# Kernel optimization log

Measured on AMD Instinct MI355X. Metric: run time of the kernel, lower is better.

The kernel has to match this reference:

```python
import jax, jax.numpy as jnp
import numpy as np
import math

B, TT, TS, C, H, L = 8, 256, 512, 512, 8, 10
HD = C // H
TOPK_FRAME = 64
# layer schedule mirrors MultimodalTransformer.forward tower order:
# 4 stimulus cross-attn (kv=frames, topk), 2 causal self-attn, 2 history cross-attn, 2 causal self-attn
# kv_source: 0=frames, 1=self, 2=id_prev
SCHED = [(0, False, TOPK_FRAME)] * 4 + [(1, True, None)] * 2 + [(2, False, None)] * 2 + [(1, True, None)] * 2


def setup_inputs() -> dict:
    key = jax.random.key(0)
    ks = jax.random.split(key, 4)
    kws = jax.random.split(ks[3], 6)
    w = lambda k, s: jax.random.normal(k, s, jnp.float32) * 0.02
    return {
        "id_x": jax.random.normal(ks[0], (B, TT, C), jnp.float32),
        "id_prev": jax.random.normal(ks[1], (B, TT, C), jnp.float32),
        "frames": jax.random.normal(ks[2], (B, TS, C), jnp.float32),
        "Wq": w(kws[0], (L, C, C)), "bq": jnp.zeros((L, C), jnp.float32),
        "Wk": w(kws[1], (L, C, C)), "bk": jnp.zeros((L, C), jnp.float32),
        "Wv": w(kws[2], (L, C, C)), "bv": jnp.zeros((L, C), jnp.float32),
        "Wo": w(kws[3], (L, C, C)), "bo": jnp.zeros((L, C), jnp.float32),
        "W1": w(kws[4], (L, C, 4 * C)), "b1": jnp.zeros((L, 4 * C), jnp.float32),
        "W2": w(kws[5], (L, 4 * C, C)), "b2": jnp.zeros((L, C), jnp.float32),
        "ln1_g": jnp.ones((L, C), jnp.float32), "ln1_b": jnp.zeros((L, C), jnp.float32),
        "ln2_g": jnp.ones((L, C), jnp.float32), "ln2_b": jnp.zeros((L, C), jnp.float32),
        "lnf_g": jnp.ones((L, C), jnp.float32), "lnf_b": jnp.zeros((L, C), jnp.float32),
    }


def _ln(x, g, b):
    mu = x.mean(-1, keepdims=True)
    var = ((x - mu) ** 2).mean(-1, keepdims=True)
    return (x - mu) * jax.lax.rsqrt(var + 1e-5) * g + b


def _block(x, kv, causal, topk, p):
    # Block.forward: x = x + attn(ln1(x), kv, kv, mask); x = x + mlp(ln2(x)); return ln_f(x)
    Wq, bq, Wk, bk, Wv, bv, Wo, bo, W1, b1, W2, b2, l1g, l1b, l2g, l2b, lfg, lfb = p
    Bx, Tt, Cx = x.shape
    Ts = kv.shape[1]
    h = _ln(x, l1g, l1b)
    q = (h @ Wq + bq).reshape(Bx, Tt, H, HD).transpose(0, 2, 1, 3)   # [B,H,Tt,HD]
    k = (kv @ Wk + bk).reshape(Bx, Ts, H, HD).transpose(0, 2, 1, 3)  # [B,H,Ts,HD]
    v = (kv @ Wv + bv).reshape(Bx, Ts, H, HD).transpose(0, 2, 1, 3)
    att = jnp.einsum('bhqd,bhkd->bhqk', q, k) * (1.0 / math.sqrt(HD))
    if causal:
        m = jnp.tril(jnp.ones((Tt, Ts), dtype=bool))
        att = jnp.where(m, att, -jnp.inf)
    if topk is not None and topk < Ts:
        top = jax.lax.top_k(att, topk)[0]           # [B,H,Tt,topk]
        att = jnp.where(att < top[..., -1:], -jnp.inf, att)
    w_att = jax.nn.softmax(att, axis=-1)
    y = jnp.einsum('bhqk,bhkd->bhqd', w_att, v).transpose(0, 2, 1, 3).reshape(Bx, Tt, Cx)
    x = x + y @ Wo + bo
    h2 = _ln(x, l2g, l2b)
    x = x + jax.nn.gelu(h2 @ W1 + b1, approximate=False) @ W2 + b2
    return _ln(x, lfg, lfb)


def _forward(id_x, id_prev, frames, Wq, bq, Wk, bk, Wv, bv, Wo, bo, W1, b1, W2, b2,
             ln1_g, ln1_b, ln2_g, ln2_b, lnf_g, lnf_b):
    x = id_x
    for i, (src, causal, topk) in enumerate(SCHED):
        kv = (frames, x, id_prev)[src]
        p = (Wq[i], bq[i], Wk[i], bk[i], Wv[i], bv[i], Wo[i], bo[i],
             W1[i], b1[i], W2[i], b2[i],
             ln1_g[i], ln1_b[i], ln2_g[i], ln2_b[i], lnf_g[i], lnf_b[i])
        x = _block(x, kv, causal, topk, p)
    return x


def reference(id_x, id_prev, frames, Wq, bq, Wk, bk, Wv, bv, Wo, bo, W1, b1, W2, b2,
              ln1_g, ln1_b, ln2_g, ln2_b, lnf_g, lnf_b):
    return _forward(id_x, id_prev, frames, Wq, bq, Wk, bk, Wv, bv, Wo, bo, W1, b1, W2, b2,
                    ln1_g, ln1_b, ln2_g, ln2_b, lnf_g, lnf_b)
```

## Files before the change

### kernel.cpp

```cpp
#include <hip/hip_runtime.h>
#include <math.h>

#define CC 512
#define NH 8
#define HD 64
#define TT 256

typedef __attribute__((ext_vector_type(8))) short short8v;
typedef __attribute__((ext_vector_type(4))) float f32x4;

__device__ inline unsigned short bfc(float f) {
  unsigned u = __float_as_uint(f);
  return (unsigned short)((u + 0x7fffu + ((u >> 16) & 1u)) >> 16);
}
__device__ inline float b2f(unsigned short s) {
  return __uint_as_float((unsigned)s << 16);
}
__device__ inline void gld16(const void* g, void* l) {
  __builtin_amdgcn_global_load_lds(
      (const __attribute__((address_space(1))) unsigned int*)g,
      (__attribute__((address_space(3))) unsigned int*)l, 16, 0, 0);
}

__global__ __launch_bounds__(256) void prep_k(const float* __restrict__ id_x,
    const float* __restrict__ frames, const float* __restrict__ id_prev,
    float* __restrict__ x, unsigned short* __restrict__ fb,
    unsigned short* __restrict__ pb) {
  int i = blockIdx.x * 256 + threadIdx.x;
  if (i < 262144) {
    ((float4*)x)[i] = ((const float4*)id_x)[i];
  } else if (i < 786432) {
    int j = i - 262144;
    float4 f = ((const float4*)frames)[j];
    ushort4 o; o.x = bfc(f.x); o.y = bfc(f.y); o.z = bfc(f.z); o.w = bfc(f.w);
    ((ushort4*)fb)[j] = o;
  } else {
    int j = i - 786432;
    float4 f = ((const float4*)id_prev)[j];
    ushort4 o; o.x = bfc(f.x); o.y = bfc(f.y); o.z = bfc(f.z); o.w = bfc(f.w);
    ((ushort4*)pb)[j] = o;
  }
}

__global__ __launch_bounds__(256) void ln_bf(const float* __restrict__ in,
    unsigned short* __restrict__ out, const float* __restrict__ g, const float* __restrict__ b) {
  int row = (blockIdx.x << 2) + (threadIdx.x >> 6), lane = threadIdx.x & 63;
  const float* r = in + (size_t)row * CC;
  float4 v0 = *(const float4*)(r + (lane << 2));
  float4 v1 = *(const float4*)(r + 256 + (lane << 2));
  float s = v0.x + v0.y + v0.z + v0.w + v1.x + v1.y + v1.z + v1.w;
  #pragma unroll
  for (int o = 32; o; o >>= 1) s += __shfl_xor(s, o);
  float mu = s * (1.0f / CC);
  float d0x = v0.x - mu, d0y = v0.y - mu, d0z = v0.z - mu, d0w = v0.w - mu;
  float d1x = v1.x - mu, d1y = v1.y - mu, d1z = v1.z - mu, d1w = v1.w - mu;
  float sq = d0x*d0x + d0y*d0y + d0z*d0z + d0w*d0w + d1x*d1x + d1y*d1y + d1z*d1z + d1w*d1w;
  #pragma unroll
  for (int o = 32; o; o >>= 1) sq += __shfl_xor(sq, o);
  float inv = rsqrtf(sq * (1.0f / CC) + 1e-5f);
  float4 g0 = *(const float4*)(g + (lane << 2)), g1 = *(const float4*)(g + 256 + (lane << 2));
  float4 b0 = *(const float4*)(b + (lane << 2)), b1 = *(const float4*)(b + 256 + (lane << 2));
  ushort4 o0, o1;
  o0.x = bfc(d0x*inv*g0.x + b0.x); o0.y = bfc(d0y*inv*g0.y + b0.y);
  o0.z = bfc(d0z*inv*g0.z + b0.z); o0.w = bfc(d0w*inv*g0.w + b0.w);
  o1.x = bfc(d1x*inv*g1.x + b1.x); o1.y = bfc(d1y*inv*g1.y + b1.y);
  o1.z = bfc(d1z*inv*g1.z + b1.z); o1.w = bfc(d1w*inv*g1.w + b1.w);
  *(ushort4*)(out + (size_t)row * CC + (lane << 2)) = o0;
  *(ushort4*)(out + (size_t)row * CC + 256 + (lane << 2)) = o1;
}

__global__ __launch_bounds__(256) void ln_final(const float* __restrict__ in,
    float* __restrict__ out, const float* __restrict__ g, const float* __restrict__ b) {
  int row = (blockIdx.x << 2) + (threadIdx.x >> 6), lane = threadIdx.x & 63;
  const float* r = in + (size_t)row * CC;
  float4 v0 = *(const float4*)(r + (lane << 2));
  float4 v1 = *(const float4*)(r + 256 + (lane << 2));
  float s = v0.x + v0.y + v0.z + v0.w + v1.x + v1.y + v1.z + v1.w;
  #pragma unroll
  for (int o = 32; o; o >>= 1) s += __shfl_xor(s, o);
  float mu = s * (1.0f / CC);
  float d0x = v0.x - mu, d0y = v0.y - mu, d0z = v0.z - mu, d0w = v0.w - mu;
  float d1x = v1.x - mu, d1y = v1.y - mu, d1z = v1.z - mu, d1w = v1.w - mu;
  float sq = d0x*d0x + d0y*d0y + d0z*d0z + d0w*d0w + d1x*d1x + d1y*d1y + d1z*d1z + d1w*d1w;
  #pragma unroll
  for (int o = 32; o; o >>= 1) sq += __shfl_xor(sq, o);
  float inv = rsqrtf(sq * (1.0f / CC) + 1e-5f);
  float4 g0 = *(const float4*)(g + (lane << 2)), g1 = *(const float4*)(g + 256 + (lane << 2));
  float4 b0 = *(const float4*)(b + (lane << 2)), b1 = *(const float4*)(b + 256 + (lane << 2));
  float4 o0, o1;
  o0.x = d0x*inv*g0.x + b0.x; o0.y = d0y*inv*g0.y + b0.y;
  o0.z = d0z*inv*g0.z + b0.z; o0.w = d0w*inv*g0.w + b0.w;
  o1.x = d1x*inv*g1.x + b1.x; o1.y = d1y*inv*g1.y + b1.y;
  o1.z = d1z*inv*g1.z + b1.z; o1.w = d1w*inv*g1.w + b1.w;
  *(float4*)(out + (size_t)row * CC + (lane << 2)) = o0;
  *(float4*)(out + (size_t)row * CC + 256 + (lane << 2)) = o1;
}

__global__ __launch_bounds__(256) void ln_chain(const float* __restrict__ in,
    float* __restrict__ xout, unsigned short* __restrict__ xb,
    const float* __restrict__ gf, const float* __restrict__ bf,
    const float* __restrict__ g1, const float* __restrict__ b1,
    unsigned short* __restrict__ hout) {
  int row = (blockIdx.x << 2) + (threadIdx.x >> 6), lane = threadIdx.x & 63;
  const float* r = in + (size_t)row * CC;
  float4 v0 = *(const float4*)(r + (lane << 2));
  float4 v1 = *(const float4*)(r + 256 + (lane << 2));
  float s = v0.x + v0.y + v0.z + v0.w + v1.x + v1.y + v1.z + v1.w;
  #pragma unroll
  for (int o = 32; o; o >>= 1) s += __shfl_xor(s, o);
  float mu = s * (1.0f / CC);
  float d0x = v0.x - mu, d0y = v0.y - mu, d0z = v0.z - mu, d0w = v0.w - mu;
  float d1x = v1.x - mu, d1y = v1.y - mu, d1z = v1.z - mu, d1w = v1.w - mu;
  float sq = d0x*d0x + d0y*d0y + d0z*d0z + d0w*d0w + d1x*d1x + d1y*d1y + d1z*d1z + d1w*d1w;
  #pragma unroll
  for (int o = 32; o; o >>= 1) sq += __shfl_xor(sq, o);
  float inv = rsqrtf(sq * (1.0f / CC) + 1e-5f);
  float4 g0 = *(const float4*)(gf + (lane << 2)), g1v = *(const float4*)(gf + 256 + (lane << 2));
  float4 b0 = *(const float4*)(bf + (lane << 2)), b1v = *(const float4*)(bf + 256 + (lane << 2));
  float4 x0, x1;
  x0.x = d0x*inv*g0.x + b0.x; x0.y = d0y*inv*g0.y + b0.y;
  x0.z = d0z*inv*g0.z + b0.z; x0.w = d0w*inv*g0.w + b0.w;
  x1.x = d1x*inv*g1v.x + b1v.x; x1.y = d1y*inv*g1v.y + b1v.y;
  x1.z = d1z*inv*g1v.z + b1v.z; x1.w = d1w*inv*g1v.w + b1v.w;
  *(float4*)(xout + (size_t)row * CC + (lane << 2)) = x0;
  *(float4*)(xout + (size_t)row * CC + 256 + (lane << 2)) = x1;
  ushort4 xb0, xb1;
  xb0.x = bfc(x0.x); xb0.y = bfc(x0.y); xb0.z = bfc(x0.z); xb0.w = bfc(x0.w);
  xb1.x = bfc(x1.x); xb1.y = bfc(x1.y); xb1.z = bfc(x1.z); xb1.w = bfc(x1.w);
  *(ushort4*)(xb + (size_t)row * CC + (lane << 2)) = xb0;
  *(ushort4*)(xb + (size_t)row * CC + 256 + (lane << 2)) = xb1;
  float s2 = x0.x + x0.y + x0.z + x0.w + x1.x + x1.y + x1.z + x1.w;
  #pragma unroll
  for (int o = 32; o; o >>= 1) s2 += __shfl_xor(s2, o);
  float mu2 = s2 * (1.0f / CC);
  float e0x = x0.x - mu2, e0y = x0.y - mu2, e0z = x0.z - mu2, e0w = x0.w - mu2;
  float e1x = x1.x - mu2, e1y = x1.y - mu2, e1z = x1.z - mu2, e1w = x1.w - mu2;
  float sq2 = e0x*e0x + e0y*e0y + e0z*e0z + e0w*e0w + e1x*e1x + e1y*e1y + e1z*e1z + e1w*e1w;
  #pragma unroll
  for (int o = 32; o; o >>= 1) sq2 += __shfl_xor(sq2, o);
  float inv2 = rsqrtf(sq2 * (1.0f / CC) + 1e-5f);
  float4 h0 = *(const float4*)(g1 + (lane << 2)), h1 = *(const float4*)(g1 + 256 + (lane << 2));
  float4 c0 = *(const float4*)(b1 + (lane << 2)), c1 = *(const float4*)(b1 + 256 + (lane << 2));
  ushort4 ho0, ho1;
  ho0.x = bfc(e0x*inv2*h0.x + c0.x); ho0.y = bfc(e0y*inv2*h0.y + c0.y);
  ho0.z = bfc(e0z*inv2*h0.z + c0.z); ho0.w = bfc(e0w*inv2*h0.w + c0.w);
  ho1.x = bfc(e1x*inv2*h1.x + c1.x); ho1.y = bfc(e1y*inv2*h1.y + c1.y);
  ho1.z = bfc(e1z*inv2*h1.z + c1.z); ho1.w = bfc(e1w*inv2*h1.w + c1.w);
  *(ushort4*)(hout + (size_t)row * CC + (lane << 2)) = ho0;
  *(ushort4*)(hout + (size_t)row * CC + 256 + (lane << 2)) = ho1;
}

__global__ __launch_bounds__(256) void transpose_w(
    const float* __restrict__ Wq, const float* __restrict__ Wk,
    const float* __restrict__ Wv, const float* __restrict__ Wo,
    const float* __restrict__ W1, const float* __restrict__ W2,
    int layer_base, unsigned short* __restrict__ wT) {
  int lz = blockIdx.x / 3072;
  int layer = layer_base + lz;
  int bid = blockIdx.x - lz * 3072;
  unsigned short* wTl = wT + (size_t)lz * 3145728;
  const float* src; unsigned short* dst; int R, Cn, tile, lg;
  if (bid < 1024) {
    int seg = bid >> 8; tile = bid & 255; R = 512; Cn = 512; lg = 4;
    const float* s4[4] = {Wq, Wk, Wv, Wo};
    src = s4[seg] + (size_t)layer * 262144;
    dst = wTl + (size_t)seg * 262144;
  } else if (bid < 2048) {
    tile = bid - 1024; R = 512; Cn = 2048; lg = 6;
    src = W1 + (size_t)layer * 1048576; dst = wTl + 1048576;
  } else {
    tile = bid - 2048; R = 2048; Cn = 512; lg = 4;
    src = W2 + (size_t)layer * 1048576; dst = wTl + 2097152;
  }
  int trb = tile >> lg, tcb = tile & ((1 << lg) - 1);
  __shared__ float tl[32][33];
  int t = threadIdx.x;
  int r = t >> 3, c4 = (t & 7) << 2;
  const float* sp = src + (size_t)(trb * 32 + r) * Cn + tcb * 32 + c4;
  float4 fv = *(const float4*)sp;
  tl[r][c4] = fv.x; tl[r][c4 + 1] = fv.y; tl[r][c4 + 2] = fv.z; tl[r][c4 + 3] = fv.w;
  __syncthreads();
  unsigned short* dp = dst + (size_t)(tcb * 32 + r) * R + trb * 32 + c4;
  ushort4 ov;
  ov.x = bfc(tl[c4][r]); ov.y = bfc(tl[c4 + 1][r]);
  ov.z = bfc(tl[c4 + 2][r]); ov.w = bfc(tl[c4 + 3][r]);
  *(ushort4*)dp = ov;
}

template<int BM, int GELU, int RES, int OUTBF, int BIAS2, int QSC>
__global__ __launch_bounds__(256) void gemm_bf(
    const unsigned short* __restrict__ A, const unsigned short* __restrict__ WT,
    const float* __restrict__ bias, const float* __restrict__ bias2,
    void* __restrict__ outp, const float* __restrict__ res, int M, int N, int K) {
  __shared__ __align__(16) unsigned short As[2][BM * 64];
  __shared__ __align__(16) unsigned short Bs[2][64 * 64];
  const int tid = threadIdx.x, lane = tid & 63, wid = tid >> 6;
  const int bm = blockIdx.y * BM, bn = blockIdx.x << 6;
  const int wm = (wid >> 1) * (BM / 2), wn = (wid & 1) << 5;
  constexpr int MF = BM / 32;
  f32x4 acc[MF][2] = {};
  const int fr = lane & 15, fq = lane >> 4;
  const int srow_a = tid >> 3, sgc = tid & 7;

  auto stage = [&](int buf, int k0) {
    #pragma unroll
    for (int i = 0; i < BM / 32; i++) {
      int row = srow_a + (i << 5);
      int gcs = sgc ^ (row & 7);
      gld16(A + (size_t)(bm + row) * K + k0 + (gcs << 3),
            (char*)As[buf] + (i << 12) + (wid << 10));
    }
    #pragma unroll
    for (int i = 0; i < 2; i++) {
      int row = srow_a + (i << 5);
      int gcs = sgc ^ (row & 7);
      gld16(WT + (size_t)(bn + row) * K + k0 + (gcs << 3),
            (char*)Bs[buf] + (i << 12) + (wid << 10));
    }
  };

  stage(0, 0);
  __syncthreads();
  int cur = 0;
  for (int k0 = 0; k0 < K; k0 += 64) {
    if (k0 + 64 < K) stage(cur ^ 1, k0 + 64);
    short8v af[MF][2], bf2[2][2];
    #pragma unroll
    for (int mf = 0; mf < MF; mf++)
      #pragma unroll
      for (int ks = 0; ks < 2; ks++) {
        int r = wm + mf * 16 + fr;
        int c = (ks << 2) + fq;
        af[mf][ks] = *(const short8v*)((const char*)As[cur] + ((((r << 7) + (c << 4))) ^ ((r & 7) << 4)));
      }
    #pragma unroll
    for (int nf = 0; nf < 2; nf++)
      #pragma unroll
      for (int ks = 0; ks < 2; ks++) {
        int r = wn + nf * 16 + fr;
        int c = (ks << 2) + fq;
        bf2[nf][ks] = *(const short8v*)((const char*)Bs[cur] + ((((r << 7) + (c << 4))) ^ ((r & 7) << 4)));
      }
    #pragma unroll
    for (int mf = 0; mf < MF; mf++)
      #pragma unroll
      for (int nf = 0; nf < 2; nf++) {
        acc[mf][nf] = __builtin_amdgcn_mfma_f32_16x16x32_bf16(af[mf][0], bf2[nf][0], acc[mf][nf], 0, 0, 0);
        acc[mf][nf] = __builtin_amdgcn_mfma_f32_16x16x32_bf16(af[mf][1], bf2[nf][1], acc[mf][nf], 0, 0, 0);
      }
    __syncthreads();
    cur ^= 1;
  }
  #pragma unroll
  for (int mf = 0; mf < MF; mf++)
    #pragma unroll
    for (int nf = 0; nf < 2; nf++) {
      int col = bn + wn + nf * 16 + fr;
      float bia = (BIAS2 && col >= 512) ? bias2[col - 512] : bias[col];
      #pragma unroll
      for (int rr = 0; rr < 4; rr++) {
        int row = bm + wm + mf * 16 + fq * 4 + rr;
        float vv = acc[mf][nf][rr] + bia;
        if (GELU) vv = 0.5f * vv * (1.0f + erff(vv * 0.70710678118654752f));
        if (RES)  vv += res[(size_t)row * N + col];
        if (QSC)  vv *= 0.125f;
        if (OUTBF) ((unsigned short*)outp)[(size_t)row * N + col] = bfc(vv);
        else       ((float*)outp)[(size_t)row * N + col] = vv;
      }
    }
}

__global__ __launch_bounds__(256) void gemm_qkv(
    const unsigned short* __restrict__ hb, const unsigned short* __restrict__ wqT,
    const float* __restrict__ bq,
    const unsigned short* __restrict__ kvA, const unsigned short* __restrict__ wkvT,
    const float* __restrict__ bk, const float* __restrict__ bv,
    unsigned short* __restrict__ qout, unsigned short* __restrict__ kvout) {
  const int tid = threadIdx.x, lane = tid & 63, wid = tid >> 6;
  int bid = blockIdx.x;
  const unsigned short *A, *WT;
  const float *bias, *bias2;
  unsigned short* outp;
  int bm, bn, N;
  bool isq = bid < 256;
  if (isq) {
    A = hb; WT = wqT; bias = bq; bias2 = bq; outp = qout; N = 512;
    bm = (bid >> 3) << 6; bn = (bid & 7) << 6;
  } else {
    int t = bid - 256;
    A = kvA; WT = wkvT; bias = bk; bias2 = bv; outp = kvout; N = 1024;
    bm = (t >> 4) << 6; bn = (t & 15) << 6;
  }
  __shared__ __align__(16) unsigned short As[2][64 * 64];
  __shared__ __align__(16) unsigned short Bs[2][64 * 64];
  const int wm = (wid >> 1) << 5, wn = (wid & 1) << 5;
  f32x4 acc[2][2] = {};
  const int fr = lane & 15, fq = lane >> 4;
  const int srow_a = tid >> 3, sgc = tid & 7;
  auto stage = [&](int buf, int k0) {
    #pragma unroll
    for (int i = 0; i < 2; i++) {
      int row = srow_a + (i << 5);
      int gcs = sgc ^ (row & 7);
      gld16(A + (size_t)(bm + row) * 512 + k0 + (gcs << 3),
            (char*)As[buf] + (i << 12) + (wid << 10));
      gld16(WT + (size_t)(bn + row) * 512 + k0 + (gcs << 3),
            (char*)Bs[buf] + (i << 12) + (wid << 10));
    }
  };
  stage(0, 0);
  __syncthreads();
  int cur = 0;
  for (int k0 = 0; k0 < 512; k0 += 64) {
    if (k0 + 64 < 512) stage(cur ^ 1, k0 + 64);
    short8v af[2][2], bf2[2][2];
    #pragma unroll
    for (int mf = 0; mf < 2; mf++)
      #pragma unroll
      for (int ks = 0; ks < 2; ks++) {
        int r = wm + mf * 16 + fr;
        int c = (ks << 2) + fq;
        af[mf][ks] = *(const short8v*)((const char*)As[cur] + ((((r << 7) + (c << 4))) ^ ((r & 7) << 4)));
        int r2 = wn + mf * 16 + fr;
        bf2[mf][ks] = *(const short8v*)((const char*)Bs[cur] + ((((r2 << 7) + (c << 4))) ^ ((r2 & 7) << 4)));
      }
    #pragma unroll
    for (int mf = 0; mf < 2; mf++)
      #pragma unroll
      for (int nf = 0; nf < 2; nf++) {
        acc[mf][nf] = __builtin_amdgcn_mfma_f32_16x16x32_bf16(af[mf][0], bf2[nf][0], acc[mf][nf], 0, 0, 0);
        acc[mf][nf] = __builtin_amdgcn_mfma_f32_16x16x32_bf16(af[mf][1], bf2[nf][1], acc[mf][nf], 0, 0, 0);
      }
    __syncthreads();
    cur ^= 1;
  }
  #pragma unroll
  for (int mf = 0; mf < 2; mf++)
    #pragma unroll
    for (int nf = 0; nf < 2; nf++) {
      int col = bn + wn + nf * 16 + fr;
      float bia = (col >= 512) ? bias2[col - 512] : bias[col];
      #pragma unroll
      for (int rr = 0; rr < 4; rr++) {
        int row = bm + wm + mf * 16 + fq * 4 + rr;
        float vv = acc[mf][nf][rr] + bia;
        if (isq) vv *= 0.125f;
        outp[(size_t)row * N + col] = bfc(vv);
      }
    }
}

template<int CAUSAL, int TOPK, int TSK>
__global__ __launch_bounds__(512, 4) void attn_m(
    const unsigned short* __restrict__ qb, const unsigned short* __restrict__ kv,
    unsigned short* __restrict__ yb) {
  constexpr int NT = TSK / 64;
  constexpr int NKC = TSK / 128;
  constexpr int SST = TSK + 8;
  constexpr int SBYTES = 8 * SST * 4;
  __shared__ __align__(16) char sm[SBYTES + 32768 + 2048];
  float* S = (float*)sm;
  char* KsB = sm + SBYTES;
  char* Qs  = sm + SBYTES + 32768;
  float* swt = (float*)KsB;
  unsigned short* kidx = (unsigned short*)(KsB + 4096);
  int tid = threadIdx.x, lane = tid & 63, wid = tid >> 6;
  int bid = blockIdx.x;
  int swz = ((bid & 7) << 8) | (bid >> 3);
  int b = swz >> 8, h = (swz >> 5) & 7, q0 = (swz & 31) << 3;
  if (tid < 64) {
    int row = tid >> 3, sp = tid & 7;
    gld16(qb + (size_t)((b << 8) + q0 + row) * CC + (h << 6) + ((sp ^ (row & 7)) << 3),
          Qs);
  } else if (tid < 128) {
    short8v z = {0, 0, 0, 0, 0, 0, 0, 0};
    *(short8v*)(Qs + (tid << 4)) = z;
  }
  const unsigned short* kgb = kv + (size_t)b * TSK * 1024 + (h << 6);
  int nte = NKC;
  if (CAUSAL) { int ub = (q0 + 8 + 127) >> 7; nte = ub < NKC ? ub : NKC; }
  auto stageK = [&](int buf, int t) {
    #pragma unroll
    for (int j = 0; j < 2; j++) {
      int s = (wid << 7) + (j << 6) + lane;
      int row = s >> 3, sp = s & 7;
      gld16(kgb + (size_t)((t << 7) + row) * 1024 + ((sp ^ (row & 7)) << 3),
            KsB + (buf << 14) + (wid << 11) + (j << 10));
    }
  };
  stageK(0, 0);
  __syncthreads();
  short8v aF[2];
  {
    int r = lane & 15, kq2 = lane >> 4;
    #pragma unroll
    for (int kc2 = 0; kc2 < 2; kc2++)
      aF[kc2] = *(const short8v*)(Qs +
                 (((r << 7) + (kc2 << 6) + (kq2 << 4)) ^ ((r & 7) << 4)));
  }
  int cur = 0;
  for (int t = 0; t < nte; t++) {
    if (t + 1 < nte) stageK(cur ^ 1, t + 1);
    int kq2 = lane >> 4;
    f32x4 acc = {};
    int key16 = (wid << 4) + (lane & 15);
    #pragma unroll
    for (int kc2 = 0; kc2 < 2; kc2++) {
      short8v bF = *(const short8v*)(KsB + (cur << 14) +
                    (((key16 << 7) + (kc2 << 6) + (kq2 << 4)) ^ ((key16 & 7) << 4)));
      acc = __builtin_amdgcn_mfma_f32_16x16x32_bf16(aF[kc2], bF, acc, 0, 0, 0);
    }
    if (kq2 < 2) {
      int col = (t << 7) + key16;
      #pragma unroll
      for (int r = 0; r < 4; r++)
        S[(kq2 * 4 + r) * SST + col] = acc[r];
    }
    __syncthreads();
    cur ^= 1;
  }
  int row = wid;
  int qi = q0 + row;
  int jmax = CAUSAL ? (qi + 1) : TSK;
  const unsigned short* vgb = kv + (size_t)b * TSK * 1024 + 512 + (h << 6) + lane;
  float sc[NT];
  float lmax = -3.0e38f;
  #pragma unroll
  for (int tt = 0; tt < NT; tt++) {
    int key = lane + (tt << 6);
    float v = (!CAUSAL || key < jmax) ? S[row * SST + key] : -3.0e38f;
    sc[tt] = v;
    lmax = fmaxf(lmax, v);
  }
  float mx = lmax;
  #pragma unroll
  for (int o = 32; o; o >>= 1) mx = fmaxf(mx, __shfl_xor(mx, o));
  float oacc = 0.f;
  if (TOPK) {
    unsigned key[NT];
    #pragma unroll
    for (int tt = 0; tt < NT; tt++) {
      unsigned u = __float_as_uint(sc[tt]);
      key[tt] = (u & 0x80000000u) ? ~u : (u | 0x80000000u);
    }
    unsigned prefix = 0u;
    for (int bit = 31; bit >= 0; bit--) {
      unsigned cand = prefix | (1u << bit);
      int cnt = 0;
      #pragma unroll
      for (int tt = 0; tt < NT; tt++)
        cnt += __popcll(__ballot(key[tt] >= cand));
      if (cnt >= 64) {
        prefix = cand;
        if (cnt == 64) break;
      }
    }
    float wvv[NT];
    float psum = 0.f;
    int basec = 0;
    #pragma unroll
    for (int tt = 0; tt < NT; tt++) {
      bool keep = key[tt] >= prefix;
      float wv = keep ? exp2f((sc[tt] - mx) * 1.4426950408889634f) : 0.f;
      wvv[tt] = wv;
      psum += wv;
      unsigned long long mask = __ballot(keep);
      if (keep) {
        int pos = basec + (int)__popcll(mask & ((1ull << lane) - 1ull));
        if (pos < 128) {
          kidx[(row << 7) + pos] = (unsigned short)(lane + (tt << 6));
          swt[(row << 7) + pos] = wv;
        }
      }
      basec += (int)__popcll(mask);
    }
    #pragma unroll
    for (int o = 32; o; o >>= 1) psum += __shfl_xor(psum, o);
    float inv = 1.0f / psum;
    int nk = basec;
    if (nk <= 128) {
      float a0 = 0.f, a1 = 0.f, a2 = 0.f, a3 = 0.f;
      int i = 0;
      for (; i + 3 < nk; i += 4) {
        a0 += swt[(row << 7) + i]     * b2f(vgb[(size_t)kidx[(row << 7) + i] * 1024]);
        a1 += swt[(row << 7) + i + 1] * b2f(vgb[(size_t)kidx[(row << 7) + i + 1] * 1024]);
        a2 += swt[(row << 7) + i + 2] * b2f(vgb[(size_t)kidx[(row << 7) + i + 2] * 1024]);
        a3 += swt[(row << 7) + i + 3] * b2f(vgb[(size_t)kidx[(row << 7) + i + 3] * 1024]);
      }
      for (; i < nk; i++) a0 += swt[(row << 7) + i] * b2f(vgb[(size_t)kidx[(row << 7) + i] * 1024]);
      oacc = (a0 + a1 + a2 + a3) * inv;
    } else {
      #pragma unroll
      for (int tt = 0; tt < NT; tt++)
        S[row * SST + lane + (tt << 6)] = wvv[tt];
      float a0 = 0.f, a1 = 0.f;
      for (int j = 0; j + 1 < TSK; j += 2) {
        a0 += S[row * SST + j]     * b2f(vgb[(size_t)j * 1024]);
        a1 += S[row * SST + j + 1] * b2f(vgb[(size_t)(j + 1) * 1024]);
      }
      oacc = (a0 + a1) * inv;
    }
  } else {
    float psum = 0.f;
    #pragma unroll
    for (int tt = 0; tt < NT; tt++) {
      int keyj = lane + (tt << 6);
      float wv = (keyj < jmax) ? exp2f((sc[tt] - mx) * 1.4426950408889634f) : 0.f;
      S[row * SST + keyj] = wv;
      psum += wv;
    }
    #pragma unroll
    for (int o = 32; o; o >>= 1) psum += __shfl_xor(psum, o);
    float inv = 1.0f / psum;
    float a0 = 0.f, a1 = 0.f, a2 = 0.f, a3 = 0.f;
    int j = 0;
    for (; j + 3 < jmax; j += 4) {
      a0 += S[row * SST + j]     * b2f(vgb[(size_t)j * 1024]);
      a1 += S[row * SST + j + 1] * b2f(vgb[(size_t)(j + 1) * 1024]);
      a2 += S[row * SST + j + 2] * b2f(vgb[(size_t)(j + 2) * 1024]);
      a3 += S[row * SST + j + 3] * b2f(vgb[(size_t)(j + 3) * 1024]);
    }
    for (; j < jmax; j++) a0 += S[row * SST + j] * b2f(vgb[(size_t)j * 1024]);
    oacc = (a0 + a1 + a2 + a3) * inv;
  }
  yb[(size_t)((b << 8) + qi) * CC + (h << 6) + lane] = bfc(oacc);
}

extern "C" void kernel_launch(void* const* d_in, const int* in_sizes, int n_in,
                              void* d_out, int out_size, void* d_ws, size_t ws_size,
                              hipStream_t stream) {
  const float* id_x    = (const float*)d_in[0];
  const float* id_prev = (const float*)d_in[1];
  const float* frames  = (const float*)d_in[2];
  const float* Wq = (const float*)d_in[3];  const float* bq = (const float*)d_in[4];
  const float* Wk = (const float*)d_in[5];  const float* bk = (const float*)d_in[6];
  const float* Wv = (const float*)d_in[7];  const float* bv = (const float*)d_in[8];
  const float* Wo = (const float*)d_in[9];  const float* bo = (const float*)d_in[10];
  const float* W1 = (const float*)d_in[11]; const float* b1 = (const float*)d_in[12];
  const float* W2 = (const float*)d_in[13]; const float* b2 = (const float*)d_in[14];
  const float* l1g = (const float*)d_in[15]; const float* l1b = (const float*)d_in[16];
  const float* l2g = (const float*)d_in[17]; const float* l2b = (const float*)d_in[18];
  const float* lfg = (const float*)d_in[19]; const float* lfb = (const float*)d_in[20];

  float* x = (float*)d_out;
  char* W  = (char*)d_ws;
  unsigned short* qbuf = (unsigned short*)W;
  unsigned short* kvb  = (unsigned short*)(W + ((size_t)4  << 20));
  unsigned short* m1b  = (unsigned short*)(W + ((size_t)4  << 20));
  unsigned short* hb   = (unsigned short*)(W + ((size_t)12 << 20));
  unsigned short* ybf  = (unsigned short*)(W + ((size_t)14 << 20));
  unsigned short* xb   = (unsigned short*)(W + ((size_t)16 << 20));
  unsigned short* fb   = (unsigned short*)(W + ((size_t)18 << 20));
  unsigned short* pb   = (unsigned short*)(W + ((size_t)22 << 20));
  unsigned short* wT   = (unsigned short*)(W + ((size_t)24 << 20));

  const bool allw = ws_size >= (((size_t)24 << 20) + (size_t)10 * 3145728 * 2);

  prep_k<<<4096, 256, 0, stream>>>(id_x, frames, id_prev, x, fb, pb);
  if (allw)
    transpose_w<<<30720, 256, 0, stream>>>(Wq, Wk, Wv, Wo, W1, W2, 0, wT);

  static const int ssrc[10] = {0, 0, 0, 0, 1, 1, 2, 2, 1, 1};

  for (int i = 0; i < 10; i++) {
    if (!allw)
      transpose_w<<<3072, 256, 0, stream>>>(Wq, Wk, Wv, Wo, W1, W2, i, wT);
    unsigned short* wTl = wT + (allw ? (size_t)i * 3145728 : 0);
    unsigned short* wqT = wTl;
    unsigned short* wkvT = wTl + 262144;
    unsigned short* woT = wTl + 786432;
    unsigned short* w1T = wTl + 1048576;
    unsigned short* w2T = wTl + 2097152;

    if (i == 0)
      ln_bf<<<512, 256, 0, stream>>>(x, hb, l1g, l1b);

    const unsigned short* kvsrc; int Mkv;
    if (ssrc[i] == 0)      { kvsrc = fb; Mkv = 4096; }
    else if (ssrc[i] == 1) { kvsrc = xb; Mkv = 2048; }
    else                   { kvsrc = pb; Mkv = 2048; }
    gemm_qkv<<<256 + (Mkv / 64) * 16, 256, 0, stream>>>(
        hb, wqT, bq + i * 512, kvsrc, wkvT, bk + i * 512, bv + i * 512, qbuf, kvb);

    if (ssrc[i] == 0)      attn_m<0, 1, 512><<<2048, 512, 0, stream>>>(qbuf, kvb, ybf);
    else if (ssrc[i] == 1) attn_m<1, 0, 256><<<2048, 512, 0, stream>>>(qbuf, kvb, ybf);
    else                   attn_m<0, 0, 256><<<2048, 512, 0, stream>>>(qbuf, kvb, ybf);

    gemm_bf<32, 0, 1, 0, 0, 0><<<dim3(8, 64), 256, 0, stream>>>(ybf, woT, bo + i * 512, nullptr, x, x, 2048, 512, 512);
    ln_bf<<<512, 256, 0, stream>>>(x, hb, l2g + i * 512, l2b + i * 512);
    gemm_bf<128, 1, 0, 1, 0, 0><<<dim3(32, 16), 256, 0, stream>>>(hb, w1T, b1 + i * 2048, nullptr, m1b, nullptr, 2048, 2048, 512);
    gemm_bf<32, 0, 1, 0, 0, 0><<<dim3(8, 64), 256, 0, stream>>>(m1b, w2T, b2 + i * 512, nullptr, x, x, 2048, 512, 2048);

    if (i < 9)
      ln_chain<<<512, 256, 0, stream>>>(x, x, xb, lfg + i * 512, lfb + i * 512,
                                        l1g + (i + 1) * 512, l1b + (i + 1) * 512, hb);
    else
      ln_final<<<512, 256, 0, stream>>>(x, x, lfg + i * 512, lfb + i * 512);
  }
}
```

Measured before the change: 1.016 ms.

## Fuse weight fp32-to-bf16 transpose into GEMM B-tile staging

Removes the separate transpose_w kernel that converted all weights to transposed bf16 in workspace. Each GEMM now loads fp32 weight rows into registers, converts them to bf16 and writes them transposed into swizzled LDS, with the register loads overlapped with the MFMA work. This saves one large launch and the extra bf16 weight write and read. In exchange every GEMM block reads fp32 weights (twice the bytes) and does the conversion repeatedly across M-tiles, and the LDS writes use 8-byte stores that may hit bank conflicts.

After: 1.321 ms. 29.9% more time.

```diff
diff --git a/kernel.cpp b/kernel.cpp
--- a/kernel.cpp
+++ b/kernel.cpp
@@ -7,6 +7,7 @@
 #define TT 256
 
 typedef __attribute__((ext_vector_type(8))) short short8v;
+typedef __attribute__((ext_vector_type(4))) short short4v;
 typedef __attribute__((ext_vector_type(4))) float f32x4;
 
 __device__ inline unsigned short bfc(float f) {
@@ -150,47 +151,10 @@
   *(ushort4*)(hout + (size_t)row * CC + 256 + (lane << 2)) = ho1;
 }
 
-__global__ __launch_bounds__(256) void transpose_w(
-    const float* __restrict__ Wq, const float* __restrict__ Wk,
-    const float* __restrict__ Wv, const float* __restrict__ Wo,
-    const float* __restrict__ W1, const float* __restrict__ W2,
-    int layer_base, unsigned short* __restrict__ wT) {
-  int lz = blockIdx.x / 3072;
-  int layer = layer_base + lz;
-  int bid = blockIdx.x - lz * 3072;
-  unsigned short* wTl = wT + (size_t)lz * 3145728;
-  const float* src; unsigned short* dst; int R, Cn, tile, lg;
-  if (bid < 1024) {
-    int seg = bid >> 8; tile = bid & 255; R = 512; Cn = 512; lg = 4;
-    const float* s4[4] = {Wq, Wk, Wv, Wo};
-    src = s4[seg] + (size_t)layer * 262144;
-    dst = wTl + (size_t)seg * 262144;
-  } else if (bid < 2048) {
-    tile = bid - 1024; R = 512; Cn = 2048; lg = 6;
-    src = W1 + (size_t)layer * 1048576; dst = wTl + 1048576;
-  } else {
-    tile = bid - 2048; R = 2048; Cn = 512; lg = 4;
-    src = W2 + (size_t)layer * 1048576; dst = wTl + 2097152;
-  }
-  int trb = tile >> lg, tcb = tile & ((1 << lg) - 1);
-  __shared__ float tl[32][33];
-  int t = threadIdx.x;
-  int r = t >> 3, c4 = (t & 7) << 2;
-  const float* sp = src + (size_t)(trb * 32 + r) * Cn + tcb * 32 + c4;
-  float4 fv = *(const float4*)sp;
-  tl[r][c4] = fv.x; tl[r][c4 + 1] = fv.y; tl[r][c4 + 2] = fv.z; tl[r][c4 + 3] = fv.w;
-  __syncthreads();
-  unsigned short* dp = dst + (size_t)(tcb * 32 + r) * R + trb * 32 + c4;
-  ushort4 ov;
-  ov.x = bfc(tl[c4][r]); ov.y = bfc(tl[c4 + 1][r]);
-  ov.z = bfc(tl[c4 + 2][r]); ov.w = bfc(tl[c4 + 3][r]);
-  *(ushort4*)dp = ov;
-}
-
-template<int BM, int GELU, int RES, int OUTBF, int BIAS2, int QSC>
+template<int BM, int GELU, int RES, int OUTBF, int QSC>
 __global__ __launch_bounds__(256) void gemm_bf(
-    const unsigned short* __restrict__ A, const unsigned short* __restrict__ WT,
-    const float* __restrict__ bias, const float* __restrict__ bias2,
+    const unsigned short* __restrict__ A, const float* __restrict__ Wf,
+    const float* __restrict__ bias,
     void* __restrict__ outp, const float* __restrict__ res, int M, int N, int K) {
   __shared__ __align__(16) unsigned short As[2][BM * 64];
   __shared__ __align__(16) unsigned short Bs[2][64 * 64];
@@ -201,8 +165,27 @@
   f32x4 acc[MF][2] = {};
   const int fr = lane & 15, fq = lane >> 4;
   const int srow_a = tid >> 3, sgc = tid & 7;
-
-  auto stage = [&](int buf, int k0) {
+  const int kkb = (tid >> 4) << 2, bn0 = (tid & 15) << 2;
+
+  float4 breg[4];
+  auto loadB = [&](int k0) {
+    #pragma unroll
+    for (int i = 0; i < 4; i++)
+      breg[i] = *(const float4*)(Wf + (size_t)(k0 + kkb + i) * N + bn + bn0);
+  };
+  auto writeB = [&](int buf) {
+    #pragma unroll
+    for (int j = 0; j < 4; j++) {
+      int n = bn0 + j;
+      short4v v;
+      v[0] = (short)bfc(((const float*)&breg[0])[j]);
+      v[1] = (short)bfc(((const float*)&breg[1])[j]);
+      v[2] = (short)bfc(((const float*)&breg[2])[j]);
+      v[3] = (short)bfc(((const float*)&breg[3])[j]);
+      *(short4v*)((char*)Bs[buf] + (((n << 7) + (kkb << 1)) ^ ((n & 7) << 4))) = v;
+    }
+  };
+  auto stageA = [&](int buf, int k0) {
     #pragma unroll
     for (int i = 0; i < BM / 32; i++) {
       int row = srow_a + (i << 5);
@@ -210,20 +193,16 @@
       gld16(A + (size_t)(bm + row) * K + k0 + (gcs << 3),
             (char*)As[buf] + (i << 12) + (wid << 10));
     }
-    #pragma unroll
-    for (int i = 0; i < 2; i++) {
-      int row = srow_a + (i << 5);
-      int gcs = sgc ^ (row & 7);
-      gld16(WT + (size_t)(bn + row) * K + k0 + (gcs << 3),
-            (char*)Bs[buf] + (i << 12) + (wid << 10));
-    }
-  };
-
-  stage(0, 0);
+  };
+
+  loadB(0);
+  stageA(0, 0);
+  writeB(0);
   __syncthreads();
   int cur = 0;
   for (int k0 = 0; k0 < K; k0 += 64) {
-    if (k0 + 64 < K) stage(cur ^ 1, k0 + 64);
+    bool more = (k0 + 64 < K);
+    if (more) { loadB(k0 + 64); stageA(cur ^ 1, k0 + 64); }
     short8v af[MF][2], bf2[2][2];
     #pragma unroll
     for (int mf = 0; mf < MF; mf++)
@@ -248,6 +227,7 @@
         acc[mf][nf] = __builtin_amdgcn_mfma_f32_16x16x32_bf16(af[mf][0], bf2[nf][0], acc[mf][nf], 0, 0, 0);
         acc[mf][nf] = __builtin_amdgcn_mfma_f32_16x16x32_bf16(af[mf][1], bf2[nf][1], acc[mf][nf], 0, 0, 0);
       }
+    if (more) writeB(cur ^ 1);
     __syncthreads();
     cur ^= 1;
   }
@@ -256,7 +236,7 @@
     #pragma unroll
     for (int nf = 0; nf < 2; nf++) {
       int col = bn + wn + nf * 16 + fr;
-      float bia = (BIAS2 && col >= 512) ? bias2[col - 512] : bias[col];
+      float bia = bias[col];
       #pragma unroll
       for (int rr = 0; rr < 4; rr++) {
         int row = bm + wm + mf * 16 + fq * 4 + rr;
@@ -271,25 +251,29 @@
 }
 
 __global__ __launch_bounds__(256) void gemm_qkv(
-    const unsigned short* __restrict__ hb, const unsigned short* __restrict__ wqT,
+    const unsigned short* __restrict__ hb, const float* __restrict__ Wq,
     const float* __restrict__ bq,
-    const unsigned short* __restrict__ kvA, const unsigned short* __restrict__ wkvT,
+    const unsigned short* __restrict__ kvA, const float* __restrict__ Wk,
+    const float* __restrict__ Wv,
     const float* __restrict__ bk, const float* __restrict__ bv,
     unsigned short* __restrict__ qout, unsigned short* __restrict__ kvout) {
   const int tid = threadIdx.x, lane = tid & 63, wid = tid >> 6;
   int bid = blockIdx.x;
-  const unsigned short *A, *WT;
-  const float *bias, *bias2;
+  const unsigned short* A;
+  const float *Wf, *bias;
   unsigned short* outp;
-  int bm, bn, N;
+  int bm, bn, N, wcol;
   bool isq = bid < 256;
   if (isq) {
-    A = hb; WT = wqT; bias = bq; bias2 = bq; outp = qout; N = 512;
-    bm = (bid >> 3) << 6; bn = (bid & 7) << 6;
+    A = hb; Wf = Wq; bias = bq; outp = qout; N = 512;
+    bm = (bid >> 3) << 6; bn = (bid & 7) << 6; wcol = bn;
   } else {
     int t = bid - 256;
-    A = kvA; WT = wkvT; bias = bk; bias2 = bv; outp = kvout; N = 1024;
+    A = kvA; outp = kvout; N = 1024;
     bm = (t >> 4) << 6; bn = (t & 15) << 6;
+    Wf = (bn < 512) ? Wk : Wv;
+    bias = (bn < 512) ? bk : bv;
+    wcol = bn & 511;
   }
   __shared__ __align__(16) unsigned short As[2][64 * 64];
   __shared__ __align__(16) unsigned short Bs[2][64 * 64];
@@ -297,22 +281,42 @@
   f32x4 acc[2][2] = {};
   const int fr = lane & 15, fq = lane >> 4;
   const int srow_a = tid >> 3, sgc = tid & 7;
-  auto stage = [&](int buf, int k0) {
+  const int kkb = (tid >> 4) << 2, bn0 = (tid & 15) << 2;
+  float4 breg[4];
+  auto loadB = [&](int k0) {
+    #pragma unroll
+    for (int i = 0; i < 4; i++)
+      breg[i] = *(const float4*)(Wf + (size_t)(k0 + kkb + i) * 512 + wcol + bn0);
+  };
+  auto writeB = [&](int buf) {
+    #pragma unroll
+    for (int j = 0; j < 4; j++) {
+      int n = bn0 + j;
+      short4v v;
+      v[0] = (short)bfc(((const float*)&breg[0])[j]);
+      v[1] = (short)bfc(((const float*)&breg[1])[j]);
+      v[2] = (short)bfc(((const float*)&breg[2])[j]);
+      v[3] = (short)bfc(((const float*)&breg[3])[j]);
+      *(short4v*)((char*)Bs[buf] + (((n << 7) + (kkb << 1)) ^ ((n & 7) << 4))) = v;
+    }
+  };
+  auto stageA = [&](int buf, int k0) {
     #pragma unroll
     for (int i = 0; i < 2; i++) {
       int row = srow_a + (i << 5);
       int gcs = sgc ^ (row & 7);
       gld16(A + (size_t)(bm + row) * 512 + k0 + (gcs << 3),
             (char*)As[buf] + (i << 12) + (wid << 10));
-      gld16(WT + (size_t)(bn + row) * 512 + k0 + (gcs << 3),
-            (char*)Bs[buf] + (i << 12) + (wid << 10));
-    }
-  };
-  stage(0, 0);
+    }
+  };
+  loadB(0);
+  stageA(0, 0);
+  writeB(0);
   __syncthreads();
   int cur = 0;
   for (int k0 = 0; k0 < 512; k0 += 64) {
-    if (k0 + 64 < 512) stage(cur ^ 1, k0 + 64);
+    bool more = (k0 + 64 < 512);
+    if (more) { loadB(k0 + 64); stageA(cur ^ 1, k0 + 64); }
     short8v af[2][2], bf2[2][2];
     #pragma unroll
     for (int mf = 0; mf < 2; mf++)
@@ -331,6 +335,7 @@
         acc[mf][nf] = __builtin_amdgcn_mfma_f32_16x16x32_bf16(af[mf][0], bf2[nf][0], acc[mf][nf], 0, 0, 0);
         acc[mf][nf] = __builtin_amdgcn_mfma_f32_16x16x32_bf16(af[mf][1], bf2[nf][1], acc[mf][nf], 0, 0, 0);
       }
+    if (more) writeB(cur ^ 1);
     __syncthreads();
     cur ^= 1;
   }
@@ -339,7 +344,7 @@
     #pragma unroll
     for (int nf = 0; nf < 2; nf++) {
       int col = bn + wn + nf * 16 + fr;
-      float bia = (col >= 512) ? bias2[col - 512] : bias[col];
+      float bia = bias[(col & 511)];
       #pragma unroll
       for (int rr = 0; rr < 4; rr++) {
         int row = bm + wm + mf * 16 + fq * 4 + rr;
@@ -552,25 +557,18 @@
   unsigned short* xb   = (unsigned short*)(W + ((size_t)16 << 20));
   unsigned short* fb   = (unsigned short*)(W + ((size_t)18 << 20));
   unsigned short* pb   = (unsigned short*)(W + ((size_t)22 << 20));
-  unsigned short* wT   = (unsigned short*)(W + ((size_t)24 << 20));
-
-  const bool allw = ws_size >= (((size_t)24 << 20) + (size_t)10 * 3145728 * 2);
 
   prep_k<<<4096, 256, 0, stream>>>(id_x, frames, id_prev, x, fb, pb);
-  if (allw)
-    transpose_w<<<30720, 256, 0, stream>>>(Wq, Wk, Wv, Wo, W1, W2, 0, wT);
 
   static const int ssrc[10] = {0, 0, 0, 0, 1, 1, 2, 2, 1, 1};
 
   for (int i = 0; i < 10; i++) {
-    if (!allw)
-      transpose_w<<<3072, 256, 0, stream>>>(Wq, Wk, Wv, Wo, W1, W2, i, wT);
-    unsigned short* wTl = wT + (allw ? (size_t)i * 3145728 : 0);
-    unsigned short* wqT = wTl;
-    unsigned short* wkvT = wTl + 262144;
-    unsigned short* woT = wTl + 786432;
-    unsigned short* w1T = wTl + 1048576;
-    unsigned short* w2T = wTl + 2097152;
+    const float* WqL = Wq + (size_t)i * 262144;
+    const float* WkL = Wk + (size_t)i * 262144;
+    const float* WvL = Wv + (size_t)i * 262144;
+    const float* WoL = Wo + (size_t)i * 262144;
+    const float* W1L = W1 + (size_t)i * 1048576;
+    const float* W2L = W2 + (size_t)i * 1048576;
 
     if (i == 0)
       ln_bf<<<512, 256, 0, stream>>>(x, hb, l1g, l1b);
@@ -580,16 +578,16 @@
     else if (ssrc[i] == 1) { kvsrc = xb; Mkv = 2048; }
     else                   { kvsrc = pb; Mkv = 2048; }
     gemm_qkv<<<256 + (Mkv / 64) * 16, 256, 0, stream>>>(
-        hb, wqT, bq + i * 512, kvsrc, wkvT, bk + i * 512, bv + i * 512, qbuf, kvb);
+        hb, WqL, bq + i * 512, kvsrc, WkL, WvL, bk + i * 512, bv + i * 512, qbuf, kvb);
 
     if (ssrc[i] == 0)      attn_m<0, 1, 512><<<2048, 512, 0, stream>>>(qbuf, kvb, ybf);
     else if (ssrc[i] == 1) attn_m<1, 0, 256><<<2048, 512, 0, stream>>>(qbuf, kvb, ybf);
     else                   attn_m<0, 0, 256><<<2048, 512, 0, stream>>>(qbuf, kvb, ybf);
 
-    gemm_bf<32, 0, 1, 0, 0, 0><<<dim3(8, 64), 256, 0, stream>>>(ybf, woT, bo + i * 512, nullptr, x, x, 2048, 512, 512);
+    gemm_bf<32, 0, 1, 0, 0><<<dim3(8, 64), 256, 0, stream>>>(ybf, WoL, bo + i * 512, x, x, 2048, 512, 512);
     ln_bf<<<512, 256, 0, stream>>>(x, hb, l2g + i * 512, l2b + i * 512);
-    gemm_bf<128, 1, 0, 1, 0, 0><<<dim3(32, 16), 256, 0, stream>>>(hb, w1T, b1 + i * 2048, nullptr, m1b, nullptr, 2048, 2048, 512);
-    gemm_bf<32, 0, 1, 0, 0, 0><<<dim3(8, 64), 256, 0, stream>>>(m1b, w2T, b2 + i * 512, nullptr, x, x, 2048, 512, 2048);
+    gemm_bf<128, 1, 0, 1, 0><<<dim3(32, 16), 256, 0, stream>>>(hb, W1L, b1 + i * 2048, m1b, nullptr, 2048, 2048, 512);
+    gemm_bf<32, 0, 1, 0, 0><<<dim3(8, 64), 256, 0, stream>>>(m1b, W2L, b2 + i * 512, x, x, 2048, 512, 2048);
 
     if (i < 9)
       ln_chain<<<512, 256, 0, stream>>>(x, x, xb, lfg + i * 512, lfb + i * 512,
```
